# Kernel tuning notes

Hardware: AMD Instinct MI355X
Metric: run time of the kernel (lower is better)

Reference implementation:

```python
import jax, jax.numpy as jnp
import numpy as np

COMMITMENT_COST = 0.25


def setup_inputs() -> dict:
    key = jax.random.key(0)
    k1, k2 = jax.random.split(key)
    x = jax.random.normal(k1, (32, 256, 32, 32), dtype=jnp.float32)          # NCHW latents
    embedding = jax.random.normal(k2, (1024, 256), dtype=jnp.float32)        # [K, D] codebook
    return {"x": x, "embedding": embedding}


def reference(x, embedding):
    # NCHW -> NHWC, flatten to [N, D]
    inp = jnp.transpose(x, (0, 2, 3, 1))
    B, H, W, D = inp.shape
    K = embedding.shape[0]
    flat = inp.reshape(-1, D)                                                # [N, D]

    dists = (jnp.sum(flat * flat, axis=1, keepdims=True)
             + jnp.sum(embedding * embedding, axis=1)
             - 2.0 * flat @ embedding.T)
    idx = jnp.argmin(dists, axis=1)                                          # [N]
    encodings = jax.nn.one_hot(idx, K, dtype=flat.dtype)                     # [N, K]

    quantized = (encodings @ embedding).reshape(B, H, W, D)

    # commitment loss (codebook detached, eval path: no EMA update)
    e_latent_loss = jnp.mean(jnp.square(jax.lax.stop_gradient(quantized) - inp))
    loss = COMMITMENT_COST * e_latent_loss

    # straight-through estimator
    quantized_st = inp + jax.lax.stop_gradient(quantized - inp)

    avg_probs = jnp.mean(encodings, axis=0)
    perplexity = jnp.exp(-jnp.sum(avg_probs * jnp.log(avg_probs + 1e-10)))

    return (loss, jnp.transpose(quantized_st, (0, 3, 1, 2)), perplexity, encodings)
```

## Files before the change

### kernel.cpp

```cpp
#include <hip/hip_runtime.h>
#include <math.h>

#define D    256
#define K    1024
#define HWX  1024
#define NPTS 32768
#define PT   64
#define NCHUNK 64

#define Q_OFF    1
#define PERP_OFF (1 + 8388608)
#define ENC_OFF  (2 + 8388608)

#define WS_FRAG_OFF 147456

typedef __attribute__((ext_vector_type(8))) short bf16x8;
typedef __attribute__((ext_vector_type(4))) float f32x4;

__device__ __forceinline__ unsigned short bf16_rne(float f) {
  unsigned int u = __float_as_uint(f);
  u = u + 0x7fffu + ((u >> 16) & 1u);
  return (unsigned short)(u >> 16);
}

#define CONV(F, H, L)                                                          \
  {                                                                            \
    H = bf16_rne(F);                                                           \
    const float fh_ = __uint_as_float((unsigned)(H) << 16);                    \
    L = bf16_rne((F)-fh_);                                                     \
  }

__global__ __launch_bounds__(256) void vq_frag(const float* __restrict__ emb,
                                               unsigned int* __restrict__ frag,
                                               float* __restrict__ enorm,
                                               int* __restrict__ counts,
                                               float* __restrict__ loss_accum) {
  const int gid = blockIdx.x * 256 + threadIdx.x;
  const int c = gid >> 5, g = gid & 31;
  const float* src = emb + (size_t)c * D + g * 8;
  const float4 a = *(const float4*)src;
  const float4 b = *(const float4*)(src + 4);
  float s = a.x * a.x + a.y * a.y + a.z * a.z + a.w * a.w +
            b.x * b.x + b.y * b.y + b.z * b.z + b.w * b.w;
#pragma unroll
  for (int off = 1; off < 32; off <<= 1) s += __shfl_xor(s, off);
  if (g == 0) enorm[c] = s;
  unsigned short h0, h1, h2, h3, h4, h5, h6, h7;
  unsigned short l0, l1, l2, l3, l4, l5, l6, l7;
  CONV(a.x, h0, l0) CONV(a.y, h1, l1) CONV(a.z, h2, l2) CONV(a.w, h3, l3)
  CONV(b.x, h4, l4) CONV(b.y, h5, l5) CONV(b.z, h6, l6) CONV(b.w, h7, l7)
  uint4 uh, ul;
  uh.x = (unsigned)h0 | ((unsigned)h1 << 16); uh.y = (unsigned)h2 | ((unsigned)h3 << 16);
  uh.z = (unsigned)h4 | ((unsigned)h5 << 16); uh.w = (unsigned)h6 | ((unsigned)h7 << 16);
  ul.x = (unsigned)l0 | ((unsigned)l1 << 16); ul.y = (unsigned)l2 | ((unsigned)l3 << 16);
  ul.z = (unsigned)l4 | ((unsigned)l5 << 16); ul.w = (unsigned)l6 | ((unsigned)l7 << 16);
  const int fragidx = (c >> 4) * 16 + (g >> 2) * 2;
  const int Lo = ((c & 15) + 16 * (g & 3)) * 4;
  *(uint4*)(frag + (size_t)fragidx * 256 + Lo) = uh;
  *(uint4*)(frag + (size_t)(fragidx + 1) * 256 + Lo) = ul;
  if (gid < K) counts[gid] = 0;
  if (gid == 0) *loss_accum = 0.0f;
}

#define ISSUE_CHUNK(P, SEL)                                                    \
  {                                                                            \
    const unsigned* gsrc = fragg + (size_t)(P)*4096 + t * 4;                   \
    unsigned short* ldst = fbuf + (SEL)*8192 + t * 8;                          \
    _Pragma("unroll") for (int q = 0; q < 4; ++q)                              \
        __builtin_amdgcn_global_load_lds(                                      \
            (const __attribute__((address_space(1))) unsigned*)(gsrc + q * 1024), \
            (__attribute__((address_space(3))) unsigned*)(ldst + q * 2048),    \
            16, 0, 0);                                                         \
  }

#define AHOIST(KSv)                                                            \
  ah##KSv = *(const bf16x8*)&fbuf[((w * 4 + ((KSv)&3)) * 2 + 0) * 512 + lane * 8]; \
  al##KSv = *(const bf16x8*)&fbuf[((w * 4 + ((KSv)&3)) * 2 + 1) * 512 + lane * 8];

#define KS3(KSv)                                                               \
  {                                                                            \
    const bf16x8 bh = *(const bf16x8*)&fbuf[bufo + ((KSv)*2 + 0) * 512 + lane * 8]; \
    const bf16x8 bl = *(const bf16x8*)&fbuf[bufo + ((KSv)*2 + 1) * 512 + lane * 8]; \
    acc = __builtin_amdgcn_mfma_f32_16x16x32_bf16(ah##KSv, bh, acc, 0, 0, 0);  \
    acc = __builtin_amdgcn_mfma_f32_16x16x32_bf16(al##KSv, bh, acc, 0, 0, 0);  \
    acc = __builtin_amdgcn_mfma_f32_16x16x32_bf16(ah##KSv, bl, acc, 0, 0, 0);  \
  }

#define STAGE_X(H)                                                             \
  {                                                                            \
    const int pt = t & 63, cb = t >> 6;                                        \
    const float* xb = x + (size_t)bb * (D * HWX) + hw0 + pt;                   \
    _Pragma("unroll 8") for (int i = 0; i < 32; ++i) {                         \
      const int c = (H)*128 + cb + 4 * i;                                      \
      const float f = xb[(size_t)c * HWX];                                     \
      unsigned short h_, l_;                                                   \
      CONV(f, h_, l_)                                                          \
      xn_acc += f * f;                                                         \
      const int ksl = (c >> 5) & 3, quad = (c >> 3) & 3, j = c & 7;            \
      const int base =                                                         \
          (((pt >> 4) * 4 + ksl) * 2) * 512 + ((pt & 15) + 16 * quad) * 8 + j; \
      fbuf[base] = h_;                                                         \
      fbuf[base + 512] = l_;                                                   \
    }                                                                          \
  }

__global__ __launch_bounds__(256) void vq_main(const float* __restrict__ x,
                                               const unsigned int* __restrict__ fragg,
                                               const float* __restrict__ emb,
                                               const float* __restrict__ enorm,
                                               float* __restrict__ out_q,
                                               float* __restrict__ out_enc,
                                               float* __restrict__ loss_accum,
                                               int* __restrict__ counts) {
  __shared__ __align__(16) unsigned short fbuf[16384];
  __shared__ float en_s[K];
  __shared__ float xn_part[256];
  __shared__ float val_s[PT];
  __shared__ int idx_s[PT];

  const int t = threadIdx.x;
  const int lane = t & 63;
  const int w = t >> 6;
  const int p0 = blockIdx.x * PT;
  const int bb = p0 >> 10;
  const int hw0 = p0 & 1023;

  bf16x8 ah0, ah1, ah2, ah3, ah4, ah5, ah6, ah7;
  bf16x8 al0, al1, al2, al3, al4, al5, al6, al7;
  float xn_acc = 0.0f;

  STAGE_X(0)
  for (int i = t; i < K; i += 256) en_s[i] = enorm[i];
  __syncthreads();
  AHOIST(0) AHOIST(1) AHOIST(2) AHOIST(3)
  __syncthreads();
  STAGE_X(1)
  xn_part[t] = xn_acc;
  __syncthreads();
  AHOIST(4) AHOIST(5) AHOIST(6) AHOIST(7)
  __syncthreads();

  float mv[4];
  int mi[4];
#pragma unroll
  for (int i = 0; i < 4; ++i) { mv[i] = 3.4e38f; mi[i] = 0; }

  ISSUE_CHUNK(0, 0)
  int sel = 0;
  for (int p = 0; p < NCHUNK; ++p) {
    __syncthreads();
    if (p + 1 < NCHUNK) ISSUE_CHUNK(p + 1, sel ^ 1)
    const int bufo = sel * 8192;
    f32x4 acc = {0.f, 0.f, 0.f, 0.f};
    KS3(0) KS3(1) KS3(2) KS3(3) KS3(4) KS3(5) KS3(6) KS3(7)
    const int code = p * 16 + (lane & 15);
    const float en_l = en_s[code];
    float m;
    m = en_l - 2.0f * acc[0]; if (m < mv[0]) { mv[0] = m; mi[0] = code; }
    m = en_l - 2.0f * acc[1]; if (m < mv[1]) { mv[1] = m; mi[1] = code; }
    m = en_l - 2.0f * acc[2]; if (m < mv[2]) { mv[2] = m; mi[2] = code; }
    m = en_l - 2.0f * acc[3]; if (m < mv[3]) { mv[3] = m; mi[3] = code; }
    sel ^= 1;
  }

#pragma unroll
  for (int off = 1; off < 16; off <<= 1) {
#pragma unroll
    for (int i = 0; i < 4; ++i) {
      const float ov = __shfl_xor(mv[i], off);
      const int oi = __shfl_xor(mi[i], off);
      if (ov < mv[i] || (ov == mv[i] && oi < mi[i])) { mv[i] = ov; mi[i] = oi; }
    }
  }
  if ((lane & 15) == 0) {
    const int quad = lane >> 4;
#pragma unroll
    for (int i = 0; i < 4; ++i) {
      val_s[w * 16 + quad * 4 + i] = mv[i];
      idx_s[w * 16 + quad * 4 + i] = mi[i];
    }
  }
  __syncthreads();
  float dist = 0.0f;
  if (t < PT) {
    float xn = 0.0f;
#pragma unroll
    for (int g = 0; g < 4; ++g) xn += xn_part[t + 64 * g];
    dist = val_s[t] + xn;
    atomicAdd(&counts[idx_s[t]], 1);
  }
  if (t < 64) {
#pragma unroll
    for (int off = 32; off > 0; off >>= 1) dist += __shfl_down(dist, off);
    if (t == 0) atomicAdd(loss_accum, dist);
  }

  float* xq = (float*)fbuf;
  for (int qd = 0; qd < 4; ++qd) {
    __syncthreads();
#pragma unroll
    for (int rr = 0; rr < 4; ++rr) {
      const int r = w * 4 + rr;
      const float4 v = ((const float4*)(emb + (size_t)idx_s[qd * 16 + r] * D))[lane];
      float* dst = &xq[r * 257 + lane];
      dst[0] = v.x; dst[64] = v.y; dst[128] = v.z; dst[192] = v.w;
    }
    __syncthreads();
    const int pt = t & 15;
    float* qb = out_q + (size_t)bb * D * HWX + hw0 + qd * 16 + pt;
#pragma unroll
    for (int ii = 0; ii < 16; ++ii) {
      const int ci = (t >> 4) + 16 * ii;
      const int pos = (ci >> 2) + 64 * (ci & 3);
      qb[(size_t)ci * HWX] = xq[pt * 257 + pos];
    }
  }
  {
    float2* eb2 = reinterpret_cast<float2*>(out_enc + (size_t)p0 * K);
#pragma unroll 4
    for (int i = t; i < PT * K / 2; i += 256) {
      const int row = i >> 9;
      const int c2 = (i & 511) * 2;
      const int target = idx_s[row];
      float2 v = make_float2(0.f, 0.f);
      if (target == c2) v.x = 1.0f;
      else if (target == c2 + 1) v.y = 1.0f;
      eb2[i] = v;
    }
  }
}

__global__ __launch_bounds__(256) void vq_final(const int* __restrict__ counts,
                                                const float* __restrict__ loss_accum,
                                                float* __restrict__ out) {
  __shared__ float sh[4];
  const int t = threadIdx.x;
  float s = 0.0f;
  for (int k = t; k < K; k += 256) {
    const float p = (float)counts[k] * (1.0f / 32768.0f);
    s += p * logf(p + 1e-10f);
  }
#pragma unroll
  for (int off = 32; off > 0; off >>= 1) s += __shfl_down(s, off);
  if ((t & 63) == 0) sh[t >> 6] = s;
  __syncthreads();
  if (t == 0) {
    const float tot = sh[0] + sh[1] + sh[2] + sh[3];
    out[PERP_OFF] = expf(-tot);
    out[0] = 0.25f * (*loss_accum) / 8388608.0f;
  }
}

extern "C" void kernel_launch(void* const* d_in, const int* in_sizes, int n_in,
                              void* d_out, int out_size, void* d_ws, size_t ws_size,
                              hipStream_t stream) {
  const float* x = (const float*)d_in[0];
  const float* emb = (const float*)d_in[1];
  float* out = (float*)d_out;
  float* enorm = (float*)d_ws;
  int* counts = (int*)((char*)d_ws + 4096);
  float* loss_accum = (float*)((char*)d_ws + 8192);
  unsigned int* fragg = (unsigned int*)((char*)d_ws + WS_FRAG_OFF);

  hipLaunchKernelGGL(vq_frag, dim3(128), dim3(256), 0, stream,
                     emb, fragg, enorm, counts, loss_accum);
  hipLaunchKernelGGL(vq_main, dim3(NPTS / PT), dim3(256), 0, stream,
                     x, fragg, emb, enorm, out + Q_OFF, out + ENC_OFF,
                     loss_accum, counts);
  hipLaunchKernelGGL(vq_final, dim3(1), dim3(256), 0, stream,
                     counts, loss_accum, out);
}
```

Before: 278.9 us.

## Triple-buffer codebook chunks and overlap one-hot zeroing with distance MFMA loop

Replaces the double-buffered codebook loop with a three-stage LDS ring that uses explicit vmcnt waits and raw barriers, so two chunks are in flight while one is computed. The one-hot encoding output is split into nontemporal zero stores issued inside the compute loop, plus a single scattered 1.0 write per row after the argmin, rather than a separate pass at the end. This aims to hide the 128MB encoding write behind the matmul. It costs more LDS (reducing occupancy) and relies on ordering between the zero stores and the later 1.0 store, which a vmcnt(0) wait before the store is meant to enforce.

```diff
diff --git a/kernel.cpp b/kernel.cpp
--- a/kernel.cpp
+++ b/kernel.cpp
@@ -16,6 +16,7 @@
 
 typedef __attribute__((ext_vector_type(8))) short bf16x8;
 typedef __attribute__((ext_vector_type(4))) float f32x4;
+typedef __attribute__((ext_vector_type(2))) float f32x2;
 
 __device__ __forceinline__ unsigned short bf16_rne(float f) {
   unsigned int u = __float_as_uint(f);
@@ -86,12 +87,35 @@
     acc = __builtin_amdgcn_mfma_f32_16x16x32_bf16(ah##KSv, bl, acc, 0, 0, 0);  \
   }
 
+#define COMPUTE_CHUNK(P, BUFO)                                                 \
+  {                                                                            \
+    const int bufo = (BUFO);                                                   \
+    f32x4 acc = {0.f, 0.f, 0.f, 0.f};                                          \
+    KS3(0) KS3(1) KS3(2) KS3(3) KS3(4) KS3(5) KS3(6) KS3(7)                    \
+    const int code = (P)*16 + (lane & 15);                                     \
+    const float en_l = en_s[code];                                             \
+    float m;                                                                   \
+    m = en_l - 2.0f * acc[0]; if (m < mv[0]) { mv[0] = m; mi[0] = code; }      \
+    m = en_l - 2.0f * acc[1]; if (m < mv[1]) { mv[1] = m; mi[1] = code; }      \
+    m = en_l - 2.0f * acc[2]; if (m < mv[2]) { mv[2] = m; mi[2] = code; }      \
+    m = en_l - 2.0f * acc[3]; if (m < mv[3]) { mv[3] = m; mi[3] = code; }      \
+  }
+
+#define ENC_ZERO(P)                                                            \
+  {                                                                            \
+    const f32x2 z_ = {0.f, 0.f};                                               \
+    __builtin_nontemporal_store(z_, encz + (P)*512 + t);                       \
+    __builtin_nontemporal_store(z_, encz + (P)*512 + 256 + t);                 \
+  }
+
+#define CFENCE asm volatile("" ::: "memory");
+
 #define STAGE_X(H)                                                             \
   {                                                                            \
-    const int pt = t & 63, cb = t >> 6;                                        \
+    const int pt = t & 63, cb_ = t >> 6;                                       \
     const float* xb = x + (size_t)bb * (D * HWX) + hw0 + pt;                   \
     _Pragma("unroll 8") for (int i = 0; i < 32; ++i) {                         \
-      const int c = (H)*128 + cb + 4 * i;                                      \
+      const int c = (H)*128 + cb_ + 4 * i;                                     \
       const float f = xb[(size_t)c * HWX];                                     \
       unsigned short h_, l_;                                                   \
       CONV(f, h_, l_)                                                          \
@@ -112,7 +136,7 @@
                                                float* __restrict__ out_enc,
                                                float* __restrict__ loss_accum,
                                                int* __restrict__ counts) {
-  __shared__ __align__(16) unsigned short fbuf[16384];
+  __shared__ __align__(16) unsigned short fbuf[24576];
   __shared__ float en_s[K];
   __shared__ float xn_part[256];
   __shared__ float val_s[PT];
@@ -145,23 +169,38 @@
 #pragma unroll
   for (int i = 0; i < 4; ++i) { mv[i] = 3.4e38f; mi[i] = 0; }
 
+  f32x2* encz = reinterpret_cast<f32x2*>(out_enc + (size_t)p0 * K);
+
   ISSUE_CHUNK(0, 0)
-  int sel = 0;
-  for (int p = 0; p < NCHUNK; ++p) {
-    __syncthreads();
-    if (p + 1 < NCHUNK) ISSUE_CHUNK(p + 1, sel ^ 1)
-    const int bufo = sel * 8192;
-    f32x4 acc = {0.f, 0.f, 0.f, 0.f};
-    KS3(0) KS3(1) KS3(2) KS3(3) KS3(4) KS3(5) KS3(6) KS3(7)
-    const int code = p * 16 + (lane & 15);
-    const float en_l = en_s[code];
-    float m;
-    m = en_l - 2.0f * acc[0]; if (m < mv[0]) { mv[0] = m; mi[0] = code; }
-    m = en_l - 2.0f * acc[1]; if (m < mv[1]) { mv[1] = m; mi[1] = code; }
-    m = en_l - 2.0f * acc[2]; if (m < mv[2]) { mv[2] = m; mi[2] = code; }
-    m = en_l - 2.0f * acc[3]; if (m < mv[3]) { mv[3] = m; mi[3] = code; }
-    sel ^= 1;
-  }
+  CFENCE
+  ISSUE_CHUNK(1, 1)
+  asm volatile("s_waitcnt vmcnt(4)" ::: "memory");
+  __builtin_amdgcn_s_barrier();
+  CFENCE
+  ENC_ZERO(0)
+  CFENCE
+  ISSUE_CHUNK(2, 2)
+  CFENCE
+  COMPUTE_CHUNK(0, 0)
+  int cb = 1;
+  for (int p = 1; p < NCHUNK - 1; ++p) {
+    asm volatile("s_waitcnt vmcnt(6)" ::: "memory");
+    __builtin_amdgcn_s_barrier();
+    CFENCE
+    ENC_ZERO(p)
+    CFENCE
+    if (p + 2 < NCHUNK) {
+      ISSUE_CHUNK(p + 2, cb == 0 ? 2 : cb - 1)
+    }
+    CFENCE
+    COMPUTE_CHUNK(p, cb * 8192)
+    cb = cb == 2 ? 0 : cb + 1;
+  }
+  asm volatile("s_waitcnt vmcnt(2)" ::: "memory");
+  __builtin_amdgcn_s_barrier();
+  CFENCE
+  ENC_ZERO(63)
+  COMPUTE_CHUNK(63, 0)
 
 #pragma unroll
   for (int off = 1; off < 16; off <<= 1) {
@@ -180,7 +219,9 @@
       idx_s[w * 16 + quad * 4 + i] = mi[i];
     }
   }
-  __syncthreads();
+  asm volatile("s_waitcnt vmcnt(0)" ::: "memory");
+  __syncthreads();
+
   float dist = 0.0f;
   if (t < PT) {
     float xn = 0.0f;
@@ -188,6 +229,7 @@
     for (int g = 0; g < 4; ++g) xn += xn_part[t + 64 * g];
     dist = val_s[t] + xn;
     atomicAdd(&counts[idx_s[t]], 1);
+    out_enc[(size_t)(p0 + t) * K + idx_s[t]] = 1.0f;
   }
   if (t < 64) {
 #pragma unroll
@@ -213,19 +255,6 @@
       const int ci = (t >> 4) + 16 * ii;
       const int pos = (ci >> 2) + 64 * (ci & 3);
       qb[(size_t)ci * HWX] = xq[pt * 257 + pos];
-    }
-  }
-  {
-    float2* eb2 = reinterpret_cast<float2*>(out_enc + (size_t)p0 * K);
-#pragma unroll 4
-    for (int i = t; i < PT * K / 2; i += 256) {
-      const int row = i >> 9;
-      const int c2 = (i & 511) * 2;
-      const int target = idx_s[row];
-      float2 v = make_float2(0.f, 0.f);
-      if (target == c2) v.x = 1.0f;
-      else if (target == c2 + 1) v.y = 1.0f;
-      eb2[i] = v;
     }
   }
 }
```

Result: faster. 264.0 us (-5.3%).
